# Kernel tuning notes

Measured on AMD Instinct MI355X. Metric: run time of the kernel, lower is better.

## Reference

```python
import jax, jax.numpy as jnp
import numpy as np

TAU = 0.1
SELF_MASK = 1e6  # added to diagonal of self-distances (y_neg is x)


def _cdist(a, b):
    # pairwise L2 distances, [Na, Nb]; eps keeps sqrt grad finite at 0
    sq = (a * a).sum(-1)[:, None] + (b * b).sum(-1)[None, :] - 2.0 * (a @ b.T)
    return jnp.sqrt(jnp.maximum(sq, 1e-12))


def setup_inputs() -> dict:
    key = jax.random.key(0)
    k1, k2 = jax.random.split(key)
    N, D = 4096, 512
    return {
        "x": jax.random.normal(k1, (N, D), dtype=jnp.float32),
        "y_pos": jax.random.normal(k2, (N, D), dtype=jnp.float32),
    }


def reference(x, y_pos):
    # compute_drift_velocity with y_neg = x (training/loss path)
    N = x.shape[0]
    dist_pos = _cdist(x, y_pos)                      # [N, N]
    dist_neg = _cdist(x, x) + SELF_MASK * jnp.eye(N, dtype=x.dtype)
    logits = -jnp.concatenate([dist_pos, dist_neg], axis=1) / TAU  # [N, 2N]
    # dual normalization: row softmax * column softmax, geometric mean
    A_row = jax.nn.softmax(logits, axis=-1)
    A_col = jax.nn.softmax(logits, axis=0)
    A = jnp.sqrt(A_row * A_col)
    A_pos, A_neg = A[:, :N], A[:, N:]
    drift = A_pos @ y_pos - A_neg @ x                # [N, D]
    return drift
```

## Files before the change

### kernel.cpp

```cpp
#include <hip/hip_runtime.h>
#include <math.h>

#define NN   4096
#define DD   512
#define TWON 8192
#define KSLICE 8

typedef _Float16 half_t;
using half8 = __attribute__((ext_vector_type(8))) half_t;
using f32x4 = __attribute__((ext_vector_type(4))) float;

__device__ __forceinline__ void gl16(const void* g, void* l) {
    __builtin_amdgcn_global_load_lds(
        (const __attribute__((address_space(1))) void*)g,
        (__attribute__((address_space(3))) void*)l, 16, 0, 0);
}
__device__ __forceinline__ f32x4 mfma16h(half8 a, half8 b, f32x4 c) {
    return __builtin_amdgcn_mfma_f32_16x16x32_f16(a, b, c, 0, 0, 0);
}

__global__ __launch_bounds__(64)
void prep_k(const float* __restrict__ x, const float* __restrict__ y,
            half_t* __restrict__ bhi, float* __restrict__ nb) {
    int r = blockIdx.x;
    int l = threadIdx.x;
    const float* src = (r < NN) ? (y + (size_t)r * DD) : (x + (size_t)(r - NN) * DD);
    float4 v0 = *reinterpret_cast<const float4*>(src + l * 8);
    float4 v1 = *reinterpret_cast<const float4*>(src + l * 8 + 4);
    float e[8] = {v0.x, v0.y, v0.z, v0.w, v1.x, v1.y, v1.z, v1.w};
    float s = 0.f;
    half8 h;
    #pragma unroll
    for (int q = 0; q < 8; ++q) {
        s += e[q] * e[q];
        h[q] = (half_t)e[q];
    }
    *reinterpret_cast<half8*>(bhi + (size_t)r * DD + l * 8) = h;
    #pragma unroll
    for (int off = 32; off; off >>= 1) s += __shfl_down(s, off);
    if (l == 0) nb[r] = s;
}

__global__ __launch_bounds__(256)
void b2t_k(const float* __restrict__ x, const float* __restrict__ y, half_t* __restrict__ b2t) {
    __shared__ float tl[32][33];
    int k0 = blockIdx.x * 32, d0 = blockIdx.y * 32;
    int tx = threadIdx.x, ty = threadIdx.y;
    const float* src = (k0 < NN) ? y : x;
    int row0 = (k0 < NN) ? k0 : (k0 - NN);
    #pragma unroll
    for (int j = 0; j < 4; ++j)
        tl[ty + 8 * j][tx] = src[(size_t)(row0 + ty + 8 * j) * DD + d0 + tx];
    __syncthreads();
    float sgn = (k0 < NN) ? 1.f : -1.f;
    #pragma unroll
    for (int j = 0; j < 4; ++j) {
        float v = tl[tx][ty + 8 * j] * sgn;
        b2t[(size_t)(d0 + ty + 8 * j) * TWON + k0 + tx] = (half_t)v;
    }
}

__global__ __launch_bounds__(256)
void gemm1_k(const half_t* __restrict__ bhi,
             const float* __restrict__ nb, half_t* __restrict__ Ef,
             float* __restrict__ rpm, float* __restrict__ rps,
             float* __restrict__ cpm, float* __restrict__ cps) {
    __shared__ unsigned char lds[32768];
    const int t = threadIdx.x;
    const int wave = t >> 6, lane = t & 63;
    const int i0 = blockIdx.y * 128, j0 = blockIdx.x * 128;
    const int wm = (wave >> 1) * 64, wn = (wave & 1) * 64;
    const half_t* ahig = bhi + (size_t)NN * DD;
    f32x4 acc[4][4] = {};
    for (int k0 = 0; k0 < DD; k0 += 64) {
        __syncthreads();
        #pragma unroll
        for (int q = 0; q < 4; ++q) {
            const int dbase = (wave * 4 + q) * 1024;
            const int p  = dbase + lane * 16;
            const int r  = p >> 7;
            const int cb = (p & 127) ^ ((r & 7) << 4);
            const size_t offA = (size_t)(i0 + r) * DD + k0 + (cb >> 1);
            const size_t offB = (size_t)(j0 + r) * DD + k0 + (cb >> 1);
            gl16(ahig + offA, lds + dbase);
            gl16(bhi  + offB, lds + 16384 + dbase);
        }
        asm volatile("s_waitcnt vmcnt(0)" ::: "memory");
        __builtin_amdgcn_sched_barrier(0);
        __syncthreads();
        #pragma unroll
        for (int kk = 0; kk < 2; ++kk) {
            half8 ah[4];
            #pragma unroll
            for (int m = 0; m < 4; ++m) {
                const int row = wm + m * 16 + (lane & 15);
                const int off = row * 128 + ((kk * 64 + (lane >> 4) * 16) ^ ((row & 7) << 4));
                ah[m] = *reinterpret_cast<const half8*>(lds + off);
            }
            #pragma unroll
            for (int n = 0; n < 4; ++n) {
                const int row = wn + n * 16 + (lane & 15);
                const int off = row * 128 + ((kk * 64 + (lane >> 4) * 16) ^ ((row & 7) << 4));
                half8 bh = *reinterpret_cast<const half8*>(lds + 16384 + off);
                #pragma unroll
                for (int m = 0; m < 4; ++m)
                    acc[m][n] = mfma16h(ah[m], bh, acc[m][n]);
            }
        }
    }
    float nbj[4];
    #pragma unroll
    for (int n = 0; n < 4; ++n) nbj[n] = nb[j0 + wn + n * 16 + (lane & 15)];
    #pragma unroll
    for (int m = 0; m < 4; ++m) {
        #pragma unroll
        for (int r4 = 0; r4 < 4; ++r4) {
            const int i = i0 + wm + m * 16 + (lane >> 4) * 4 + r4;
            const float nxi = nb[NN + i];
            #pragma unroll
            for (int n = 0; n < 4; ++n) {
                const int j = j0 + wn + n * 16 + (lane & 15);
                float sq = nxi + nbj[n] - 2.0f * acc[m][n][r4];
                float lg = -10.0f * sqrtf(fmaxf(sq, 1e-12f));
                if (j == i + NN) lg = -1e7f;
                acc[m][n][r4] = lg;
            }
        }
    }
    float rmx[16];
    #pragma unroll
    for (int m = 0; m < 4; ++m)
        #pragma unroll
        for (int r4 = 0; r4 < 4; ++r4)
            rmx[m * 4 + r4] = fmaxf(fmaxf(acc[m][0][r4], acc[m][1][r4]),
                                    fmaxf(acc[m][2][r4], acc[m][3][r4]));
    #pragma unroll
    for (int off = 1; off < 16; off <<= 1)
        #pragma unroll
        for (int idx = 0; idx < 16; ++idx)
            rmx[idx] = fmaxf(rmx[idx], __shfl_xor(rmx[idx], off));
    __syncthreads();
    float* red = reinterpret_cast<float*>(lds);
    if ((lane & 15) == 0) {
        #pragma unroll
        for (int m = 0; m < 4; ++m)
            #pragma unroll
            for (int r4 = 0; r4 < 4; ++r4) {
                const int r = wm + m * 16 + (lane >> 4) * 4 + r4;
                red[(wave & 1) * 128 + r] = rmx[m * 4 + r4];
            }
    }
    __syncthreads();
    float rmt[16];
    #pragma unroll
    for (int m = 0; m < 4; ++m)
        #pragma unroll
        for (int r4 = 0; r4 < 4; ++r4) {
            const int r = wm + m * 16 + (lane >> 4) * 4 + r4;
            rmt[m * 4 + r4] = fmaxf(rmx[m * 4 + r4], red[(((wave & 1) ^ 1)) * 128 + r]);
        }
    float rs[16] = {};
    #pragma unroll
    for (int m = 0; m < 4; ++m) {
        #pragma unroll
        for (int r4 = 0; r4 < 4; ++r4) {
            const int idx = m * 4 + r4;
            const int i = i0 + wm + m * 16 + (lane >> 4) * 4 + r4;
            #pragma unroll
            for (int n = 0; n < 4; ++n) {
                const int j = j0 + wn + n * 16 + (lane & 15);
                float e = __expf(acc[m][n][r4] - rmt[idx]);
                acc[m][n][r4] = e;
                Ef[(size_t)i * TWON + j] = (half_t)(e * 1024.0f);
                rs[idx] += e;
            }
        }
    }
    #pragma unroll
    for (int off = 1; off < 16; off <<= 1)
        #pragma unroll
        for (int idx = 0; idx < 16; ++idx) rs[idx] += __shfl_xor(rs[idx], off);
    float tmax = rmt[0];
    #pragma unroll
    for (int idx = 1; idx < 16; ++idx) tmax = fmaxf(tmax, rmt[idx]);
    tmax = fmaxf(tmax, __shfl_xor(tmax, 16));
    tmax = fmaxf(tmax, __shfl_xor(tmax, 32));
    __syncthreads();
    if (((wave & 1) == 0) && (lane & 15) == 0) {
        #pragma unroll
        for (int m = 0; m < 4; ++m)
            #pragma unroll
            for (int r4 = 0; r4 < 4; ++r4) {
                const int r = wm + m * 16 + (lane >> 4) * 4 + r4;
                red[r] = rmt[m * 4 + r4];
            }
    }
    if ((lane & 15) == 0) {
        #pragma unroll
        for (int m = 0; m < 4; ++m)
            #pragma unroll
            for (int r4 = 0; r4 < 4; ++r4) {
                const int r = wm + m * 16 + (lane >> 4) * 4 + r4;
                red[128 + (wave & 1) * 128 + r] = rs[m * 4 + r4];
            }
    }
    if (lane == 0) red[384 + wave] = tmax;
    __syncthreads();
    const float C = fmaxf(fmaxf(red[384], red[385]), fmaxf(red[386], red[387]));
    float w[16];
    #pragma unroll
    for (int idx = 0; idx < 16; ++idx) w[idx] = __expf(rmt[idx] - C);
    float cs[4] = {};
    #pragma unroll
    for (int m = 0; m < 4; ++m)
        #pragma unroll
        for (int r4 = 0; r4 < 4; ++r4)
            #pragma unroll
            for (int n = 0; n < 4; ++n)
                cs[n] = fmaf(acc[m][n][r4], w[m * 4 + r4], cs[n]);
    #pragma unroll
    for (int off = 16; off < 64; off <<= 1)
        #pragma unroll
        for (int n = 0; n < 4; ++n) cs[n] += __shfl_xor(cs[n], off);
    if (lane < 16) {
        #pragma unroll
        for (int n = 0; n < 4; ++n) {
            const int c = wn + n * 16 + lane;
            red[512 + (wave >> 1) * 128 + c] = cs[n];
        }
    }
    __syncthreads();
    if (t < 128) {
        rpm[(size_t)blockIdx.x * NN + i0 + t] = red[t];
        rps[(size_t)blockIdx.x * NN + i0 + t] = red[128 + t] + red[256 + t];
    } else {
        const int c = t - 128;
        cpm[(size_t)blockIdx.y * TWON + j0 + c] = C;
        cps[(size_t)blockIdx.y * TWON + j0 + c] = red[512 + c] + red[640 + c];
    }
}

__global__ __launch_bounds__(256)
void row_comb_k(const float* __restrict__ rpm, const float* __restrict__ rps,
                float* __restrict__ rm, float* __restrict__ rrs) {
    int i = blockIdx.x * 256 + threadIdx.x;
    float M = -3.0e38f;
    for (int tt = 0; tt < TWON / 128; ++tt) M = fmaxf(M, rpm[(size_t)tt * NN + i]);
    float S = 0.f;
    for (int tt = 0; tt < TWON / 128; ++tt)
        S += rps[(size_t)tt * NN + i] * __expf(rpm[(size_t)tt * NN + i] - M);
    rm[i] = M; rrs[i] = rsqrtf(S);
}

__global__ __launch_bounds__(256)
void col_comb_k(const float* __restrict__ cpm, const float* __restrict__ cps,
                float* __restrict__ Pj) {
    int j = blockIdx.x * 256 + threadIdx.x;
    float M = -3.0e38f;
    for (int tt = 0; tt < NN / 128; ++tt) M = fmaxf(M, cpm[(size_t)tt * TWON + j]);
    float S = 0.f;
    for (int tt = 0; tt < NN / 128; ++tt)
        S += cps[(size_t)tt * TWON + j] * __expf(cpm[(size_t)tt * TWON + j] - M);
    Pj[j] = -0.5f * M - 0.5f * logf(S);
}

__global__ __launch_bounds__(512, 4)
void gemm2_k(const half_t* __restrict__ Ef, const half_t* __restrict__ b2t,
             const float* __restrict__ rpm, const float* __restrict__ rm,
             const float* __restrict__ Pj, const float* __restrict__ rrs,
             float* __restrict__ part) {
    __shared__ unsigned char lds[16384];
    const int t = threadIdx.x;
    const int wave = t >> 6, lane = t & 63;
    const int sw = blockIdx.x;
    const int kslice = sw & 7;
    const int i0 = (sw >> 3) * 64;
    const int kbase = kslice * (TWON / KSLICE);
    const int wn = wave * 64;
    const int sr = t >> 3;
    const int kc = (t & 7) * 8;
    const int awbyte = sr * 128 + ((kc * 2) ^ ((sr & 7) << 4));
    const int NT = (TWON / KSLICE) / 64;
    const float rmh = 0.5f * rm[i0 + sr] + 6.9314718f;
    f32x4 acc[4][4] = {};
    half8 aE;
    float4 p0, p1;
    float arg;
    auto LOADA = [&](int it) {
        const int k = kbase + it * 64 + kc;
        aE = *reinterpret_cast<const half8*>(Ef + (size_t)(i0 + sr) * TWON + k);
        p0 = *reinterpret_cast<const float4*>(Pj + k);
        p1 = *reinterpret_cast<const float4*>(Pj + k + 4);
        arg = rpm[(size_t)((kbase + it * 64) >> 7) * NN + i0 + sr] - rmh;
    };
    auto STOREA = [&](int buf) {
        half8 g;
        g[0] = (half_t)((float)aE[0] * __expf(arg + p0.x));
        g[1] = (half_t)((float)aE[1] * __expf(arg + p0.y));
        g[2] = (half_t)((float)aE[2] * __expf(arg + p0.z));
        g[3] = (half_t)((float)aE[3] * __expf(arg + p0.w));
        g[4] = (half_t)((float)aE[4] * __expf(arg + p1.x));
        g[5] = (half_t)((float)aE[5] * __expf(arg + p1.y));
        g[6] = (half_t)((float)aE[6] * __expf(arg + p1.z));
        g[7] = (half_t)((float)aE[7] * __expf(arg + p1.w));
        *reinterpret_cast<half8*>(lds + buf * 8192 + awbyte) = g;
    };
    LOADA(0);
    STOREA(0);
    __syncthreads();
    int cur = 0;
    for (int it = 0; it < NT; ++it) {
        half8 bfr0[4], bfr1[4];
        #pragma unroll
        for (int n = 0; n < 4; ++n) {
            const int d = wn + n * 16 + (lane & 15);
            const half_t* bp = b2t + (size_t)d * TWON + kbase + it * 64 + (lane >> 4) * 8;
            bfr0[n] = *reinterpret_cast<const half8*>(bp);
            bfr1[n] = *reinterpret_cast<const half8*>(bp + 32);
        }
        if (it + 1 < NT) LOADA(it + 1);
        #pragma unroll
        for (int kk = 0; kk < 2; ++kk) {
            half8 af[4];
            #pragma unroll
            for (int m = 0; m < 4; ++m) {
                const int row = m * 16 + (lane & 15);
                const int off = cur * 8192 + row * 128 +
                                ((kk * 64 + (lane >> 4) * 16) ^ ((row & 7) << 4));
                af[m] = *reinterpret_cast<const half8*>(lds + off);
            }
            #pragma unroll
            for (int m = 0; m < 4; ++m)
                #pragma unroll
                for (int n = 0; n < 4; ++n)
                    acc[m][n] = mfma16h(af[m], (kk == 0) ? bfr0[n] : bfr1[n], acc[m][n]);
        }
        if (it + 1 < NT) STOREA(cur ^ 1);
        __syncthreads();
        cur ^= 1;
    }
    float* pout = part + (size_t)kslice * NN * DD;
    #pragma unroll
    for (int m = 0; m < 4; ++m) {
        float rf[4];
        #pragma unroll
        for (int r4 = 0; r4 < 4; ++r4) rf[r4] = rrs[i0 + m * 16 + (lane >> 4) * 4 + r4];
        #pragma unroll
        for (int n = 0; n < 4; ++n) {
            const int d = wn + n * 16 + (lane & 15);
            #pragma unroll
            for (int r4 = 0; r4 < 4; ++r4) {
                const int i = i0 + m * 16 + (lane >> 4) * 4 + r4;
                pout[(size_t)i * DD + d] = acc[m][n][r4] * rf[r4];
            }
        }
    }
}

__global__ __launch_bounds__(256)
void reduce_k(const float* __restrict__ part, float* __restrict__ out) {
    const size_t e4 = ((size_t)blockIdx.x * 256 + threadIdx.x) * 4;
    float4 a = *reinterpret_cast<const float4*>(part + e4);
    #pragma unroll
    for (int s = 1; s < KSLICE; ++s) {
        float4 b = *reinterpret_cast<const float4*>(part + (size_t)s * NN * DD + e4);
        a.x += b.x; a.y += b.y; a.z += b.z; a.w += b.w;
    }
    *reinterpret_cast<float4*>(out + e4) = a;
}

extern "C" void kernel_launch(void* const* d_in, const int* in_sizes, int n_in,
                              void* d_out, int out_size, void* d_ws, size_t ws_size,
                              hipStream_t stream) {
    const float* x = (const float*)d_in[0];
    const float* y = (const float*)d_in[1];
    float* out = (float*)d_out;

    char* w = (char*)d_ws;
    const size_t OFF_EF   = 0;
    const size_t OFF_BHI  = 67108864;
    const size_t OFF_B2T  = OFF_BHI + 8388608;
    const size_t OFF_PART = OFF_B2T + 8388608;
    const size_t OFF_RPM  = OFF_PART + 67108864;
    const size_t OFF_RPS  = OFF_RPM + 1048576;
    const size_t OFF_CPM  = OFF_RPS + 1048576;
    const size_t OFF_CPS  = OFF_CPM + 1048576;
    const size_t OFF_TAIL = OFF_CPS + 1048576;

    half_t* Ef   = (half_t*)(w + OFF_EF);
    half_t* bhi  = (half_t*)(w + OFF_BHI);
    half_t* b2t  = (half_t*)(w + OFF_B2T);
    float*  part = (float*)(w + OFF_PART);
    float*  rpm  = (float*)(w + OFF_RPM);
    float*  rps  = (float*)(w + OFF_RPS);
    float*  cpm  = (float*)(w + OFF_CPM);
    float*  cps  = (float*)(w + OFF_CPS);
    float*  nb   = (float*)(w + OFF_TAIL);
    float*  rm   = nb  + TWON;
    float*  rrs  = rm  + NN;
    float*  Pj   = rrs + NN;

    prep_k<<<TWON, 64, 0, stream>>>(x, y, bhi, nb);
    gemm1_k<<<dim3(TWON / 128, NN / 128), 256, 0, stream>>>(bhi, nb, Ef,
                                                            rpm, rps, cpm, cps);
    row_comb_k<<<NN / 256, 256, 0, stream>>>(rpm, rps, rm, rrs);
    col_comb_k<<<TWON / 256, 256, 0, stream>>>(cpm, cps, Pj);
    b2t_k<<<dim3(TWON / 32, DD / 32), dim3(32, 8), 0, stream>>>(x, y, b2t);
    gemm2_k<<<512, 512, 0, stream>>>(Ef, b2t, rpm, rm, Pj, rrs, part);
    reduce_k<<<(NN * DD / 4) / 256, 256, 0, stream>>>(part, out);
}
```

Before: 195.9 us.

## Use per-tile max with bf16 storage to simplify softmax epilogue

Result: faster. 188.8 us (-3.6%).

```diff
diff --git a/kernel.cpp b/kernel.cpp
--- a/kernel.cpp
+++ b/kernel.cpp
@@ -7,9 +7,19 @@
 #define KSLICE 8
 
 typedef _Float16 half_t;
-using half8 = __attribute__((ext_vector_type(8))) half_t;
-using f32x4 = __attribute__((ext_vector_type(4))) float;
-
+typedef unsigned short u16;
+using half8  = __attribute__((ext_vector_type(8))) half_t;
+using short8 = __attribute__((ext_vector_type(8))) short;
+using f32x4  = __attribute__((ext_vector_type(4))) float;
+
+__device__ __forceinline__ u16 f2bf(float f) {
+    unsigned u = __float_as_uint(f);
+    u += 0x7fffu + ((u >> 16) & 1u);
+    return (u16)(u >> 16);
+}
+__device__ __forceinline__ float bf2f(u16 h) {
+    return __uint_as_float(((unsigned)h) << 16);
+}
 __device__ __forceinline__ void gl16(const void* g, void* l) {
     __builtin_amdgcn_global_load_lds(
         (const __attribute__((address_space(1))) void*)g,
@@ -17,6 +27,9 @@
 }
 __device__ __forceinline__ f32x4 mfma16h(half8 a, half8 b, f32x4 c) {
     return __builtin_amdgcn_mfma_f32_16x16x32_f16(a, b, c, 0, 0, 0);
+}
+__device__ __forceinline__ f32x4 mfma16b(short8 a, short8 b, f32x4 c) {
+    return __builtin_amdgcn_mfma_f32_16x16x32_bf16(a, b, c, 0, 0, 0);
 }
 
 __global__ __launch_bounds__(64)
@@ -42,7 +55,7 @@
 }
 
 __global__ __launch_bounds__(256)
-void b2t_k(const float* __restrict__ x, const float* __restrict__ y, half_t* __restrict__ b2t) {
+void b2t_k(const float* __restrict__ x, const float* __restrict__ y, u16* __restrict__ b2t) {
     __shared__ float tl[32][33];
     int k0 = blockIdx.x * 32, d0 = blockIdx.y * 32;
     int tx = threadIdx.x, ty = threadIdx.y;
@@ -56,13 +69,14 @@
     #pragma unroll
     for (int j = 0; j < 4; ++j) {
         float v = tl[tx][ty + 8 * j] * sgn;
-        b2t[(size_t)(d0 + ty + 8 * j) * TWON + k0 + tx] = (half_t)v;
+        b2t[(size_t)(d0 + ty + 8 * j) * TWON + k0 + tx] = f2bf(v);
     }
 }
 
 __global__ __launch_bounds__(256)
 void gemm1_k(const half_t* __restrict__ bhi,
-             const float* __restrict__ nb, half_t* __restrict__ Ef,
+             const float* __restrict__ nb, u16* __restrict__ Ef,
+             float* __restrict__ Ct,
              float* __restrict__ rpm, float* __restrict__ rps,
              float* __restrict__ cpm, float* __restrict__ cps) {
     __shared__ unsigned char lds[32768];
@@ -111,6 +125,7 @@
     float nbj[4];
     #pragma unroll
     for (int n = 0; n < 4; ++n) nbj[n] = nb[j0 + wn + n * 16 + (lane & 15)];
+    float tmax = -3.0e38f;
     #pragma unroll
     for (int m = 0; m < 4; ++m) {
         #pragma unroll
@@ -124,44 +139,22 @@
                 float lg = -10.0f * sqrtf(fmaxf(sq, 1e-12f));
                 if (j == i + NN) lg = -1e7f;
                 acc[m][n][r4] = lg;
-            }
-        }
-    }
-    float rmx[16];
+                tmax = fmaxf(tmax, lg);
+            }
+        }
+    }
+    #pragma unroll
+    for (int off = 1; off < 64; off <<= 1) tmax = fmaxf(tmax, __shfl_xor(tmax, off));
+    __syncthreads();
+    float* red = reinterpret_cast<float*>(lds);
+    if (lane == 0) red[wave] = tmax;
+    __syncthreads();
+    const float C = fmaxf(fmaxf(red[0], red[1]), fmaxf(red[2], red[3]));
+    __syncthreads();
+    if (t == 0) Ct[blockIdx.y * 64 + blockIdx.x] = C;
+    float rs[16] = {}, cs[4] = {};
     #pragma unroll
     for (int m = 0; m < 4; ++m)
-        #pragma unroll
-        for (int r4 = 0; r4 < 4; ++r4)
-            rmx[m * 4 + r4] = fmaxf(fmaxf(acc[m][0][r4], acc[m][1][r4]),
-                                    fmaxf(acc[m][2][r4], acc[m][3][r4]));
-    #pragma unroll
-    for (int off = 1; off < 16; off <<= 1)
-        #pragma unroll
-        for (int idx = 0; idx < 16; ++idx)
-            rmx[idx] = fmaxf(rmx[idx], __shfl_xor(rmx[idx], off));
-    __syncthreads();
-    float* red = reinterpret_cast<float*>(lds);
-    if ((lane & 15) == 0) {
-        #pragma unroll
-        for (int m = 0; m < 4; ++m)
-            #pragma unroll
-            for (int r4 = 0; r4 < 4; ++r4) {
-                const int r = wm + m * 16 + (lane >> 4) * 4 + r4;
-                red[(wave & 1) * 128 + r] = rmx[m * 4 + r4];
-            }
-    }
-    __syncthreads();
-    float rmt[16];
-    #pragma unroll
-    for (int m = 0; m < 4; ++m)
-        #pragma unroll
-        for (int r4 = 0; r4 < 4; ++r4) {
-            const int r = wm + m * 16 + (lane >> 4) * 4 + r4;
-            rmt[m * 4 + r4] = fmaxf(rmx[m * 4 + r4], red[(((wave & 1) ^ 1)) * 128 + r]);
-        }
-    float rs[16] = {};
-    #pragma unroll
-    for (int m = 0; m < 4; ++m) {
         #pragma unroll
         for (int r4 = 0; r4 < 4; ++r4) {
             const int idx = m * 4 + r4;
@@ -169,74 +162,48 @@
             #pragma unroll
             for (int n = 0; n < 4; ++n) {
                 const int j = j0 + wn + n * 16 + (lane & 15);
-                float e = __expf(acc[m][n][r4] - rmt[idx]);
-                acc[m][n][r4] = e;
-                Ef[(size_t)i * TWON + j] = (half_t)(e * 1024.0f);
+                float e = __expf(acc[m][n][r4] - C);
+                Ef[(size_t)i * TWON + j] = f2bf(e);
                 rs[idx] += e;
-            }
-        }
-    }
-    #pragma unroll
-    for (int off = 1; off < 16; off <<= 1)
+                cs[n]   += e;
+            }
+        }
+    #pragma unroll
+    for (int off = 1; off < 16; off <<= 1) {
         #pragma unroll
         for (int idx = 0; idx < 16; ++idx) rs[idx] += __shfl_xor(rs[idx], off);
-    float tmax = rmt[0];
-    #pragma unroll
-    for (int idx = 1; idx < 16; ++idx) tmax = fmaxf(tmax, rmt[idx]);
-    tmax = fmaxf(tmax, __shfl_xor(tmax, 16));
-    tmax = fmaxf(tmax, __shfl_xor(tmax, 32));
-    __syncthreads();
-    if (((wave & 1) == 0) && (lane & 15) == 0) {
+    }
+    #pragma unroll
+    for (int off = 16; off < 64; off <<= 1) {
+        #pragma unroll
+        for (int n = 0; n < 4; ++n) cs[n] += __shfl_xor(cs[n], off);
+    }
+    if ((lane & 15) == 0) {
         #pragma unroll
         for (int m = 0; m < 4; ++m)
             #pragma unroll
             for (int r4 = 0; r4 < 4; ++r4) {
                 const int r = wm + m * 16 + (lane >> 4) * 4 + r4;
-                red[r] = rmt[m * 4 + r4];
-            }
-    }
-    if ((lane & 15) == 0) {
-        #pragma unroll
-        for (int m = 0; m < 4; ++m)
-            #pragma unroll
-            for (int r4 = 0; r4 < 4; ++r4) {
-                const int r = wm + m * 16 + (lane >> 4) * 4 + r4;
-                red[128 + (wave & 1) * 128 + r] = rs[m * 4 + r4];
-            }
-    }
-    if (lane == 0) red[384 + wave] = tmax;
-    __syncthreads();
-    const float C = fmaxf(fmaxf(red[384], red[385]), fmaxf(red[386], red[387]));
-    float w[16];
-    #pragma unroll
-    for (int idx = 0; idx < 16; ++idx) w[idx] = __expf(rmt[idx] - C);
-    float cs[4] = {};
-    #pragma unroll
-    for (int m = 0; m < 4; ++m)
-        #pragma unroll
-        for (int r4 = 0; r4 < 4; ++r4)
-            #pragma unroll
-            for (int n = 0; n < 4; ++n)
-                cs[n] = fmaf(acc[m][n][r4], w[m * 4 + r4], cs[n]);
-    #pragma unroll
-    for (int off = 16; off < 64; off <<= 1)
-        #pragma unroll
-        for (int n = 0; n < 4; ++n) cs[n] += __shfl_xor(cs[n], off);
+                red[(wave & 1) * 128 + r] = rs[m * 4 + r4];
+            }
+    }
     if (lane < 16) {
         #pragma unroll
         for (int n = 0; n < 4; ++n) {
             const int c = wn + n * 16 + lane;
-            red[512 + (wave >> 1) * 128 + c] = cs[n];
+            red[256 + (wave >> 1) * 128 + c] = cs[n];
         }
     }
     __syncthreads();
     if (t < 128) {
-        rpm[(size_t)blockIdx.x * NN + i0 + t] = red[t];
-        rps[(size_t)blockIdx.x * NN + i0 + t] = red[128 + t] + red[256 + t];
+        float S = red[t] + red[128 + t];
+        rpm[(size_t)blockIdx.x * NN + i0 + t] = C;
+        rps[(size_t)blockIdx.x * NN + i0 + t] = S;
     } else {
         const int c = t - 128;
+        float S = red[256 + c] + red[384 + c];
         cpm[(size_t)blockIdx.y * TWON + j0 + c] = C;
-        cps[(size_t)blockIdx.y * TWON + j0 + c] = red[512 + c] + red[640 + c];
+        cps[(size_t)blockIdx.y * TWON + j0 + c] = S;
     }
 }
 
@@ -265,8 +232,8 @@
 }
 
 __global__ __launch_bounds__(512, 4)
-void gemm2_k(const half_t* __restrict__ Ef, const half_t* __restrict__ b2t,
-             const float* __restrict__ rpm, const float* __restrict__ rm,
+void gemm2_k(const u16* __restrict__ Ef, const u16* __restrict__ b2t,
+             const float* __restrict__ Ct, const float* __restrict__ rm,
              const float* __restrict__ Pj, const float* __restrict__ rrs,
              float* __restrict__ part) {
     __shared__ unsigned char lds[16384];
@@ -275,65 +242,66 @@
     const int sw = blockIdx.x;
     const int kslice = sw & 7;
     const int i0 = (sw >> 3) * 64;
+    const int ib = (sw >> 3) >> 1;
     const int kbase = kslice * (TWON / KSLICE);
     const int wn = wave * 64;
     const int sr = t >> 3;
     const int kc = (t & 7) * 8;
     const int awbyte = sr * 128 + ((kc * 2) ^ ((sr & 7) << 4));
     const int NT = (TWON / KSLICE) / 64;
-    const float rmh = 0.5f * rm[i0 + sr] + 6.9314718f;
+    const float rmh = 0.5f * rm[i0 + sr];
     f32x4 acc[4][4] = {};
-    half8 aE;
+    short8 aE;
     float4 p0, p1;
     float arg;
     auto LOADA = [&](int it) {
         const int k = kbase + it * 64 + kc;
-        aE = *reinterpret_cast<const half8*>(Ef + (size_t)(i0 + sr) * TWON + k);
+        aE = *reinterpret_cast<const short8*>(Ef + (size_t)(i0 + sr) * TWON + k);
         p0 = *reinterpret_cast<const float4*>(Pj + k);
         p1 = *reinterpret_cast<const float4*>(Pj + k + 4);
-        arg = rpm[(size_t)((kbase + it * 64) >> 7) * NN + i0 + sr] - rmh;
+        arg = Ct[ib * 64 + ((kbase + it * 64) >> 7)] - rmh;
     };
     auto STOREA = [&](int buf) {
-        half8 g;
-        g[0] = (half_t)((float)aE[0] * __expf(arg + p0.x));
-        g[1] = (half_t)((float)aE[1] * __expf(arg + p0.y));
-        g[2] = (half_t)((float)aE[2] * __expf(arg + p0.z));
-        g[3] = (half_t)((float)aE[3] * __expf(arg + p0.w));
-        g[4] = (half_t)((float)aE[4] * __expf(arg + p1.x));
-        g[5] = (half_t)((float)aE[5] * __expf(arg + p1.y));
-        g[6] = (half_t)((float)aE[6] * __expf(arg + p1.z));
-        g[7] = (half_t)((float)aE[7] * __expf(arg + p1.w));
-        *reinterpret_cast<half8*>(lds + buf * 8192 + awbyte) = g;
+        short8 g;
+        g[0] = (short)f2bf(bf2f((u16)aE[0]) * __expf(arg + p0.x));
+        g[1] = (short)f2bf(bf2f((u16)aE[1]) * __expf(arg + p0.y));
+        g[2] = (short)f2bf(bf2f((u16)aE[2]) * __expf(arg + p0.z));
+        g[3] = (short)f2bf(bf2f((u16)aE[3]) * __expf(arg + p0.w));
+        g[4] = (short)f2bf(bf2f((u16)aE[4]) * __expf(arg + p1.x));
+        g[5] = (short)f2bf(bf2f((u16)aE[5]) * __expf(arg + p1.y));
+        g[6] = (short)f2bf(bf2f((u16)aE[6]) * __expf(arg + p1.z));
+        g[7] = (short)f2bf(bf2f((u16)aE[7]) * __expf(arg + p1.w));
+        *reinterpret_cast<short8*>(lds + buf * 8192 + awbyte) = g;
     };
     LOADA(0);
     STOREA(0);
     __syncthreads();
     int cur = 0;
     for (int it = 0; it < NT; ++it) {
-        half8 bfr0[4], bfr1[4];
+        short8 bfr0[4], bfr1[4];
         #pragma unroll
         for (int n = 0; n < 4; ++n) {
             const int d = wn + n * 16 + (lane & 15);
-            const half_t* bp = b2t + (size_t)d * TWON + kbase + it * 64 + (lane >> 4) * 8;
-            bfr0[n] = *reinterpret_cast<const half8*>(bp);
-            bfr1[n] = *reinterpret_cast<const half8*>(bp + 32);
+            const u16* bp = b2t + (size_t)d * TWON + kbase + it * 64 + (lane >> 4) * 8;
+            bfr0[n] = *reinterpret_cast<const short8*>(bp);
+            bfr1[n] = *reinterpret_cast<const short8*>(bp + 32);
         }
         if (it + 1 < NT) LOADA(it + 1);
         #pragma unroll
         for (int kk = 0; kk < 2; ++kk) {
-            half8 af[4];
+            short8 af[4];
             #pragma unroll
             for (int m = 0; m < 4; ++m) {
                 const int row = m * 16 + (lane & 15);
                 const int off = cur * 8192 + row * 128 +
                                 ((kk * 64 + (lane >> 4) * 16) ^ ((row & 7) << 4));
-                af[m] = *reinterpret_cast<const half8*>(lds + off);
+                af[m] = *reinterpret_cast<const short8*>(lds + off);
             }
             #pragma unroll
             for (int m = 0; m < 4; ++m)
                 #pragma unroll
                 for (int n = 0; n < 4; ++n)
-                    acc[m][n] = mfma16h(af[m], (kk == 0) ? bfr0[n] : bfr1[n], acc[m][n]);
+                    acc[m][n] = mfma16b(af[m], (kk == 0) ? bfr0[n] : bfr1[n], acc[m][n]);
         }
         if (it + 1 < NT) STOREA(cur ^ 1);
         __syncthreads();
@@ -385,27 +353,29 @@
     const size_t OFF_RPS  = OFF_RPM + 1048576;
     const size_t OFF_CPM  = OFF_RPS + 1048576;
     const size_t OFF_CPS  = OFF_CPM + 1048576;
-    const size_t OFF_TAIL = OFF_CPS + 1048576;
-
-    half_t* Ef   = (half_t*)(w + OFF_EF);
+    const size_t OFF_CT   = OFF_CPS + 1048576;
+    const size_t OFF_TAIL = OFF_CT + 65536;
+
+    u16*    Ef   = (u16*)(w + OFF_EF);
     half_t* bhi  = (half_t*)(w + OFF_BHI);
-    half_t* b2t  = (half_t*)(w + OFF_B2T);
+    u16*    b2t  = (u16*)(w + OFF_B2T);
     float*  part = (float*)(w + OFF_PART);
     float*  rpm  = (float*)(w + OFF_RPM);
     float*  rps  = (float*)(w + OFF_RPS);
     float*  cpm  = (float*)(w + OFF_CPM);
     float*  cps  = (float*)(w + OFF_CPS);
+    float*  Ct   = (float*)(w + OFF_CT);
     float*  nb   = (float*)(w + OFF_TAIL);
     float*  rm   = nb  + TWON;
     float*  rrs  = rm  + NN;
     float*  Pj   = rrs + NN;
 
     prep_k<<<TWON, 64, 0, stream>>>(x, y, bhi, nb);
-    gemm1_k<<<dim3(TWON / 128, NN / 128), 256, 0, stream>>>(bhi, nb, Ef,
+    gemm1_k<<<dim3(TWON / 128, NN / 128), 256, 0, stream>>>(bhi, nb, Ef, Ct,
                                                             rpm, rps, cpm, cps);
     row_comb_k<<<NN / 256, 256, 0, stream>>>(rpm, rps, rm, rrs);
     col_comb_k<<<TWON / 256, 256, 0, stream>>>(cpm, cps, Pj);
     b2t_k<<<dim3(TWON / 32, DD / 32), dim3(32, 8), 0, stream>>>(x, y, b2t);
-    gemm2_k<<<512, 512, 0, stream>>>(Ef, b2t, rpm, rm, Pj, rrs, part);
+    gemm2_k<<<512, 512, 0, stream>>>(Ef, b2t, Ct, rm, Pj, rrs, part);
     reduce_k<<<(NN * DD / 4) / 256, 256, 0, stream>>>(part, out);
 }
```
